# Optimization experiments

Measured on AMD Instinct MI355X. Metric: run time of the kernel, lower is better.

The kernel has to match this reference:

```python
import jax, jax.numpy as jnp
import numpy as np

NUM_HEADS = 16

def setup_inputs() -> dict:
    key = jax.random.key(0)
    ks = jax.random.split(key, 5)
    B, N, C = 2, 2048, 1024
    x = jax.random.normal(ks[0], (B, N, C), dtype=jnp.float32)
    s_in = 1.0 / np.sqrt(C)
    Wq = jax.random.normal(ks[1], (C, 2 * C), dtype=jnp.float32) * s_in
    Wk = jax.random.normal(ks[2], (C, 2 * C), dtype=jnp.float32) * s_in
    Wv = jax.random.normal(ks[3], (C, 2 * C), dtype=jnp.float32) * s_in
    Wo = jax.random.normal(ks[4], (2 * C, C), dtype=jnp.float32) * (1.0 / np.sqrt(2 * C))
    return {"x": x, "Wq": Wq, "Wk": Wk, "Wv": Wv, "Wo": Wo}

def reference(x, Wq, Wk, Wv, Wo):
    B, N, C = x.shape
    H = NUM_HEADS
    hd = C // H  # head_dim
    def proj(W):
        # [B,N,2C] -> [B,H,N,2*hd]
        return (x @ W).reshape(B, N, H, 2 * hd).transpose(0, 2, 1, 3)
    q = proj(Wq)
    k = proj(Wk)
    v = proj(Wv)
    q_r, q_i = q[..., :hd], q[..., hd:]
    k_r, k_i = k[..., :hd], k[..., hd:]
    v_r, v_i = v[..., :hd], v[..., hd:]
    # complex inner product real part: Re(Q K^H) = q_r.k_r + q_i.k_i
    scores = (jnp.einsum('bhnd,bhmd->bhnm', q_r, k_r)
              + jnp.einsum('bhnd,bhmd->bhnm', q_i, k_i)) / jnp.sqrt(jnp.float32(hd))
    causal = jnp.tril(jnp.ones((N, N), dtype=bool))  # [N,N]
    scores = jnp.where(causal[None, None], scores, -jnp.inf)
    probs = jax.nn.softmax(scores, axis=-1)  # dropout off (eval mode)
    out_r = jnp.einsum('bhnm,bhmd->bhnd', probs, v_r)
    out_i = jnp.einsum('bhnm,bhmd->bhnd', probs, v_i)
    out = jnp.concatenate([out_r, out_i], axis=-1)  # [B,H,N,2*hd]
    out = out.transpose(0, 2, 1, 3).reshape(B, N, 2 * C)
    return out @ Wo  # [B,N,C]
```

## Files before the change

### kernel.cpp

```cpp
#include <hip/hip_runtime.h>
#include <hip/hip_bf16.h>
#include <stdint.h>
#include <cmath>

using bf16 = __hip_bfloat16;
typedef __attribute__((ext_vector_type(8))) short bf16x8;
typedef __attribute__((ext_vector_type(4))) short bf16x4;
typedef __attribute__((ext_vector_type(4))) float f32x4;

#define MFMA16(a, b, c) __builtin_amdgcn_mfma_f32_16x16x32_bf16(a, b, c, 0, 0, 0)

#if defined(__has_builtin)
#if __has_builtin(__builtin_amdgcn_mfma_f32_16x16x16bf16_1k)
#define HAVE_MFMA_K16 1
#endif
#if __has_builtin(__builtin_amdgcn_exp2f)
#define EXP2F __builtin_amdgcn_exp2f
#endif
#endif
#ifndef HAVE_MFMA_K16
#define HAVE_MFMA_K16 0
#endif
#ifndef EXP2F
#define EXP2F exp2f
#endif

#define NEG_BIG (-1e30f)
#define K2SCALE 0.18033688011112042f

__device__ __forceinline__ short f2bf(float v) {
  return __builtin_bit_cast(short, __float2bfloat16(v));
}

__device__ __forceinline__ f32x4 pv_mfma(bf16x4 va, bf16x4 pb, f32x4 c) {
#if HAVE_MFMA_K16
  return __builtin_amdgcn_mfma_f32_16x16x16bf16_1k(va, pb, c, 0, 0, 0);
#else
  const bf16x8 a = {va[0], va[1], va[2], va[3], 0, 0, 0, 0};
  const bf16x8 b = {pb[0], pb[1], pb[2], pb[3], 0, 0, 0, 0};
  return MFMA16(a, b, c);
#endif
}

__device__ __forceinline__ void async_ld16(const bf16* g, bf16* l) {
  __builtin_amdgcn_global_load_lds(
      (const __attribute__((address_space(1))) unsigned int*)g,
      (__attribute__((address_space(3))) unsigned int*)l, 16, 0, 0);
}

template <typename T> __device__ __forceinline__ T cvt_out(float v);
template <> __device__ __forceinline__ float cvt_out<float>(float v) { return v; }
template <> __device__ __forceinline__ bf16 cvt_out<bf16>(float v) { return __float2bfloat16(v); }

__global__ void prep(const float* __restrict__ x,
                     const float* __restrict__ Wq, const float* __restrict__ Wk,
                     const float* __restrict__ Wv, const float* __restrict__ Wo,
                     bf16* __restrict__ xb, bf16* __restrict__ tq,
                     bf16* __restrict__ tk, bf16* __restrict__ tv,
                     bf16* __restrict__ to_) {
  __shared__ bf16 tile[32][33];
  const int bid = blockIdx.x;
  if (bid < 8192) {
    const int z = bid >> 11, tt = bid & 2047;
    const float* in = z == 0 ? Wq : z == 1 ? Wk : z == 2 ? Wv : Wo;
    bf16* out = z == 0 ? tq : z == 1 ? tk : z == 2 ? tv : to_;
    int R, Cc, c0, r0;
    if (z < 3) { R = 1024; Cc = 2048; c0 = (tt & 63) * 32; r0 = (tt >> 6) * 32; }
    else       { R = 2048; Cc = 1024; c0 = (tt & 31) * 32; r0 = (tt >> 5) * 32; }
    const int xx = threadIdx.x & 31;
    const int y = threadIdx.x >> 5;
#pragma unroll
    for (int yy = y; yy < 32; yy += 8)
      tile[yy][xx] = __float2bfloat16(in[(size_t)(r0 + yy) * Cc + c0 + xx]);
    __syncthreads();
#pragma unroll
    for (int yy = y; yy < 32; yy += 8)
      out[(size_t)(c0 + yy) * R + r0 + xx] = tile[xx][yy];
  } else {
    const int i = (bid - 8192) * 256 + threadIdx.x;
    const float4 v = ((const float4*)x)[i];
    bf16 o[4] = {__float2bfloat16(v.x), __float2bfloat16(v.y),
                 __float2bfloat16(v.z), __float2bfloat16(v.w)};
    *(uint64_t*)&xb[i * 4] = *(const uint64_t*)o;
  }
}

__global__ __launch_bounds__(256)
void gemm_qkv(const bf16* __restrict__ xb, const bf16* __restrict__ wq,
              const bf16* __restrict__ wk, const bf16* __restrict__ wv,
              bf16* __restrict__ qo, bf16* __restrict__ ko, bf16* __restrict__ vo) {
  __shared__ __align__(16) bf16 As[128 * 32];
  __shared__ __align__(16) bf16 Bs[128 * 32];
  const int op = blockIdx.y;
  const int bid = blockIdx.x;
  const bf16 *A, *B;
  int m0, n0;
  if (op < 2) { A = xb; B = op ? wk : wq; m0 = (bid >> 4) * 128; n0 = (bid & 15) * 128; }
  else        { A = wv; B = xb;           m0 = (bid & 15) * 128; n0 = (bid >> 4) * 128; }
  const int K = 1024;

  const int t = threadIdx.x;
  const int l = t & 63, w = t >> 6;
  const int q4 = l >> 4, li = l & 15;
  const int wr = (w >> 1) * 64, wc = (w & 1) * 64;

  f32x4 acc[4][4] = {};
  const int colst = (t & 3) * 8;
  const bf16* gA = A + (size_t)m0 * K;
  const bf16* gB = B + (size_t)n0 * K;

  for (int k0 = 0; k0 < K; k0 += 32) {
#pragma unroll
    for (int p = 0; p < 2; ++p) {
      const int row = p * 64 + (t >> 2);
      const int lbase = p * 2048 + (t & ~63) * 8;
      async_ld16(gA + (size_t)row * K + k0 + colst, &As[lbase]);
      async_ld16(gB + (size_t)row * K + k0 + colst, &Bs[lbase]);
    }
    __syncthreads();
    bf16x8 af[4], bfr[4];
#pragma unroll
    for (int i = 0; i < 4; ++i)
      af[i] = *(const bf16x8*)&As[(wr + i * 16 + li) * 32 + q4 * 8];
#pragma unroll
    for (int j = 0; j < 4; ++j)
      bfr[j] = *(const bf16x8*)&Bs[(wc + j * 16 + li) * 32 + q4 * 8];
#pragma unroll
    for (int i = 0; i < 4; ++i)
#pragma unroll
      for (int j = 0; j < 4; ++j)
        acc[i][j] = MFMA16(af[i], bfr[j], acc[i][j]);
    __syncthreads();
  }

#pragma unroll
  for (int i = 0; i < 4; ++i)
#pragma unroll
    for (int j = 0; j < 4; ++j)
#pragma unroll
      for (int r = 0; r < 4; ++r) {
        const int gm = m0 + wr + i * 16 + q4 * 4 + r;
        const int gn = n0 + wc + j * 16 + li;
        const bf16 v = __float2bfloat16(acc[i][j][r]);
        if (op < 2) {
          const int b = gm >> 11, nn = gm & 2047;
          const int h = gn >> 7, d = gn & 127;
          (op ? ko : qo)[((size_t)(b * 16 + h) * 2048 + nn) * 128 + d] = v;
        } else {
          const int h = gm >> 7, d = gm & 127;
          const int b = gn >> 11, nn = gn & 2047;
          vo[((size_t)(b * 16 + h) * 128 + d) * 2048 + nn] = v;
        }
      }
}

template <int NT, typename OT>
__global__ __launch_bounds__(256)
void gemm_bt(const bf16* __restrict__ A, const bf16* __restrict__ B,
             OT* __restrict__ C, int M, int N, int K) {
  __shared__ __align__(16) bf16 As[128 * 32];
  __shared__ __align__(16) bf16 Bs[NT * 32];
  constexpr int JN = NT / 32;
  const int t = threadIdx.x;
  const int l = t & 63, w = t >> 6;
  const int q4 = l >> 4, li = l & 15;
  const int m0 = blockIdx.y * 128;
  const int n0 = blockIdx.x * NT;
  const int wr = (w >> 1) * 64, wc = (w & 1) * (NT / 2);

  f32x4 acc[4][JN] = {};
  const int colst = (t & 3) * 8;
  const bf16* gA = A + (size_t)m0 * K;
  const bf16* gB = B + (size_t)n0 * K;

  for (int k0 = 0; k0 < K; k0 += 32) {
#pragma unroll
    for (int p = 0; p < 2; ++p) {
      const int row = p * 64 + (t >> 2);
      const int lbase = p * 2048 + (t & ~63) * 8;
      async_ld16(gA + (size_t)row * K + k0 + colst, &As[lbase]);
    }
#pragma unroll
    for (int p = 0; p < NT / 64; ++p) {
      const int row = p * 64 + (t >> 2);
      const int lbase = p * 2048 + (t & ~63) * 8;
      async_ld16(gB + (size_t)row * K + k0 + colst, &Bs[lbase]);
    }
    __syncthreads();
    bf16x8 af[4], bfr[JN];
#pragma unroll
    for (int i = 0; i < 4; ++i)
      af[i] = *(const bf16x8*)&As[(wr + i * 16 + li) * 32 + q4 * 8];
#pragma unroll
    for (int j = 0; j < JN; ++j)
      bfr[j] = *(const bf16x8*)&Bs[(wc + j * 16 + li) * 32 + q4 * 8];
#pragma unroll
    for (int i = 0; i < 4; ++i)
#pragma unroll
      for (int j = 0; j < JN; ++j)
        acc[i][j] = MFMA16(af[i], bfr[j], acc[i][j]);
    __syncthreads();
  }

#pragma unroll
  for (int i = 0; i < 4; ++i)
#pragma unroll
    for (int j = 0; j < JN; ++j)
#pragma unroll
      for (int r = 0; r < 4; ++r) {
        const int gm = m0 + wr + i * 16 + q4 * 4 + r;
        const int gn = n0 + wc + j * 16 + li;
        C[(size_t)gm * N + gn] = cvt_out<OT>(acc[i][j][r]);
      }
}

__global__ __launch_bounds__(256, 2)
void flash_attn(const bf16* __restrict__ qm, const bf16* __restrict__ km,
                const bf16* __restrict__ vtm, bf16* __restrict__ om) {
  __shared__ __align__(16) bf16 Ks[128 * 128];
  __shared__ __align__(16) bf16 Vts[128 * 128];

  const int t = threadIdx.x;
  const int l = t & 63, w = t >> 6;
  const int q4 = l >> 4, li = l & 15;
  const int bh = blockIdx.x;
  const int y = blockIdx.y;
  const int qt = (y < 8) ? 15 - y : y - 8;
  const int qs = qt * 128;
  const size_t qkbase = (size_t)bh * 2048 * 128;
  const size_t vbase = (size_t)bh * 128 * 2048;
  const int b = bh >> 4, h = bh & 15;

  bf16x8 qf[2][4];
#pragma unroll
  for (int g = 0; g < 2; ++g) {
    const bf16* Qb = qm + qkbase + (size_t)(qs + w * 32 + g * 16 + li) * 128;
#pragma unroll
    for (int f = 0; f < 4; ++f)
      qf[g][f] = *(const bf16x8*)(Qb + f * 32 + q4 * 8);
  }

  f32x4 O[2][8] = {};
  float mrun[2] = {NEG_BIG, NEG_BIG}, lrun[2] = {0.f, 0.f};
  const int gmq[2] = {qs + w * 32 + li, qs + w * 32 + 16 + li};

  const int srow = t >> 4;
  const int wavebase = (t & ~63) * 8;

  for (int kt = 0; kt <= qt; ++kt) {
    const int kn = kt * 128;
#pragma unroll
    for (int p = 0; p < 8; ++p) {
      const int row = p * 16 + srow;
      const int cs = (t & 15) ^ (row & 7);
      const int ldsoff = p * 2048 + wavebase;
      async_ld16(km + qkbase + (size_t)(kn + row) * 128 + cs * 8, &Ks[ldsoff]);
      async_ld16(vtm + vbase + (size_t)row * 2048 + kn + cs * 8, &Vts[ldsoff]);
    }
    __syncthreads();

    const bool diag = (kt == qt);
#pragma unroll
    for (int half = 0; half < 2; ++half) {
      const int kb = kn + half * 64;
      if (diag && (qs + w * 32 + 31) < kb) continue;

      f32x4 S[2][4];
#pragma unroll
      for (int jk = 0; jk < 4; ++jk) {
        const int krow = half * 64 + jk * 16 + li;
        bf16x8 kf[4];
#pragma unroll
        for (int f = 0; f < 4; ++f)
          kf[f] = *(const bf16x8*)&Ks[krow * 128 + (((f * 4 + q4) ^ (li & 7)) * 8)];
#pragma unroll
        for (int g = 0; g < 2; ++g) {
          f32x4 s = {0.f, 0.f, 0.f, 0.f};
#pragma unroll
          for (int f = 0; f < 4; ++f) s = MFMA16(kf[f], qf[g][f], s);
          S[g][jk] = s;
        }
      }

      bf16x4 pb[2][4];
      float mold[2], nmv[2], rsv[2];
      bool nomove = true;
#pragma unroll
      for (int g = 0; g < 2; ++g) {
        if (diag) {
#pragma unroll
          for (int jk = 0; jk < 4; ++jk)
#pragma unroll
            for (int r = 0; r < 4; ++r)
              if ((kb + jk * 16 + q4 * 4 + r) > gmq[g]) S[g][jk][r] = NEG_BIG;
        }
        float mx = NEG_BIG;
#pragma unroll
        for (int jk = 0; jk < 4; ++jk)
          mx = fmaxf(mx, fmaxf(fmaxf(S[g][jk][0], S[g][jk][1]),
                               fmaxf(S[g][jk][2], S[g][jk][3])));
        mx = fmaxf(mx, __shfl_xor(mx, 16));
        mx = fmaxf(mx, __shfl_xor(mx, 32));
        mold[g] = mrun[g];
        const float nm = fmaxf(mrun[g], mx);
        nomove = nomove && (mx <= mold[g]);
        mrun[g] = nm;
        nmv[g] = nm;
        const float nmk = nm * K2SCALE;
        float rs = 0.f;
#pragma unroll
        for (int jk = 0; jk < 4; ++jk)
#pragma unroll
          for (int r = 0; r < 4; ++r) {
            const float e = EXP2F(__builtin_fmaf(S[g][jk][r], K2SCALE, -nmk));
            rs += e;
            pb[g][jk][r] = f2bf(e);
          }
        rs += __shfl_xor(rs, 16);
        rs += __shfl_xor(rs, 32);
        rsv[g] = rs;
      }

      if (__all(nomove)) {
        lrun[0] += rsv[0];
        lrun[1] += rsv[1];
      } else {
#pragma unroll
        for (int g = 0; g < 2; ++g) {
          const float alpha = EXP2F((mold[g] - nmv[g]) * K2SCALE);
          lrun[g] = lrun[g] * alpha + rsv[g];
#pragma unroll
          for (int dt = 0; dt < 8; ++dt) O[g][dt] *= alpha;
        }
      }

#pragma unroll
      for (int dt = 0; dt < 8; ++dt)
#pragma unroll
        for (int kc = 0; kc < 4; ++kc) {
          const int gchunk = half * 8 + kc * 2 + (q4 >> 1);
          const bf16x4 va = *(const bf16x4*)&Vts[(dt * 16 + li) * 128 +
                                                 ((gchunk ^ (li & 7)) * 8) +
                                                 (q4 & 1) * 4];
          O[0][dt] = pv_mfma(va, pb[0][kc], O[0][dt]);
          O[1][dt] = pv_mfma(va, pb[1][kc], O[1][dt]);
        }
    }
    __syncthreads();
  }

#pragma unroll
  for (int g = 0; g < 2; ++g) {
    const float inv = 1.0f / lrun[g];
    const size_t orow = (size_t)(b * 2048 + qs + w * 32 + g * 16 + li) * 2048 + h * 128;
#pragma unroll
    for (int dt = 0; dt < 8; ++dt) {
      bf16x4 o4;
#pragma unroll
      for (int r = 0; r < 4; ++r) o4[r] = f2bf(O[g][dt][r] * inv);
      *(bf16x4*)&om[orow + dt * 16 + q4 * 4] = o4;
    }
  }
}

extern "C" void kernel_launch(void* const* d_in, const int* in_sizes, int n_in,
                              void* d_out, int out_size, void* d_ws, size_t ws_size,
                              hipStream_t stream) {
  const float* x = (const float*)d_in[0];
  const float* Wq = (const float*)d_in[1];
  const float* Wk = (const float*)d_in[2];
  const float* Wv = (const float*)d_in[3];
  const float* Wo = (const float*)d_in[4];
  float* out = (float*)d_out;

  bf16* ws = (bf16*)d_ws;
  const size_t MEG = 1u << 20;
  bf16* xb = ws;
  bf16* wTq = ws + 4 * MEG;
  bf16* wTk = ws + 6 * MEG;
  bf16* wTv = ws + 8 * MEG;
  bf16* woT = ws + 10 * MEG;
  bf16* at_ws = ws + 2 * MEG;
  bf16* q_ws = ws + 12 * MEG;
  bf16* k_ws = ws + 20 * MEG;
  bf16* vt_ws = ws + 28 * MEG;

  const dim3 blk(256);

  prep<<<dim3(12288), blk, 0, stream>>>(x, Wq, Wk, Wv, Wo, xb, wTq, wTk, wTv, woT);
  gemm_qkv<<<dim3(512, 3), blk, 0, stream>>>(xb, wTq, wTk, wTv, q_ws, k_ws, vt_ws);
  flash_attn<<<dim3(32, 16), blk, 0, stream>>>(q_ws, k_ws, vt_ws, at_ws);
  gemm_bt<64, float><<<dim3(16, 32), blk, 0, stream>>>(at_ws, woT, out, 4096, 1024, 2048);
}
```

Measured before the change: 273.9 us.

## Double-buffer 64-key K/V tiles to overlap global loads with attention compute

Splits each 128-key KV tile into 64-key tiles held in two LDS buffers, so the async loads for the next tile are issued while the current tile is being computed. The old code issued all loads and then waited at a barrier, leaving compute idle. LDS footprint stays the same, but there are twice as many barriers, and the V tile indexing and swizzle now use a 64-column layout.

Result: slower. 280.7 us (+2.5%).

```diff
diff --git a/kernel.cpp b/kernel.cpp
--- a/kernel.cpp
+++ b/kernel.cpp
@@ -217,8 +217,8 @@
 __global__ __launch_bounds__(256, 2)
 void flash_attn(const bf16* __restrict__ qm, const bf16* __restrict__ km,
                 const bf16* __restrict__ vtm, bf16* __restrict__ om) {
-  __shared__ __align__(16) bf16 Ks[128 * 128];
-  __shared__ __align__(16) bf16 Vts[128 * 128];
+  __shared__ __align__(16) bf16 Ks[2][64 * 128];
+  __shared__ __align__(16) bf16 Vts[2][128 * 64];
 
   const int t = threadIdx.x;
   const int l = t & 63, w = t >> 6;
@@ -244,35 +244,60 @@
   float mrun[2] = {NEG_BIG, NEG_BIG}, lrun[2] = {0.f, 0.f};
   const int gmq[2] = {qs + w * 32 + li, qs + w * 32 + 16 + li};
 
-  const int srow = t >> 4;
+  const int ksrow = t >> 4;
+  const int kchu = t & 15;
+  const int vsrow = t >> 3;
+  const int vchu = t & 7;
   const int wavebase = (t & ~63) * 8;
 
-  for (int kt = 0; kt <= qt; ++kt) {
-    const int kn = kt * 128;
-#pragma unroll
-    for (int p = 0; p < 8; ++p) {
-      const int row = p * 16 + srow;
-      const int cs = (t & 15) ^ (row & 7);
-      const int ldsoff = p * 2048 + wavebase;
-      async_ld16(km + qkbase + (size_t)(kn + row) * 128 + cs * 8, &Ks[ldsoff]);
-      async_ld16(vtm + vbase + (size_t)row * 2048 + kn + cs * 8, &Vts[ldsoff]);
-    }
-    __syncthreads();
-
-    const bool diag = (kt == qt);
-#pragma unroll
-    for (int half = 0; half < 2; ++half) {
-      const int kb = kn + half * 64;
-      if (diag && (qs + w * 32 + 31) < kb) continue;
+  const int nt = 2 * qt + 2;
+
+  {
+#pragma unroll
+    for (int p = 0; p < 4; ++p) {
+      const int kr = p * 16 + ksrow;
+      async_ld16(km + qkbase + (size_t)kr * 128 + (size_t)((kchu ^ (kr & 7)) * 8),
+                 &Ks[0][p * 2048 + wavebase]);
+      const int vr = p * 32 + vsrow;
+      async_ld16(vtm + vbase + (size_t)vr * 2048 + (size_t)((vchu ^ (vr & 7)) * 8),
+                 &Vts[0][p * 2048 + wavebase]);
+    }
+  }
+  asm volatile("s_waitcnt vmcnt(0)" ::: "memory");
+  __builtin_amdgcn_s_barrier();
+  asm volatile("" ::: "memory");
+
+  int cur = 0;
+  for (int j = 0; j < nt; ++j, cur ^= 1) {
+    if (j + 1 < nt) {
+      const int kn = (j + 1) * 64;
+      bf16* kd = &Ks[cur ^ 1][0];
+      bf16* vd = &Vts[cur ^ 1][0];
+#pragma unroll
+      for (int p = 0; p < 4; ++p) {
+        const int kr = p * 16 + ksrow;
+        async_ld16(km + qkbase + (size_t)(kn + kr) * 128 + (size_t)((kchu ^ (kr & 7)) * 8),
+                   kd + p * 2048 + wavebase);
+        const int vr = p * 32 + vsrow;
+        async_ld16(vtm + vbase + (size_t)vr * 2048 + kn + (size_t)((vchu ^ (vr & 7)) * 8),
+                   vd + p * 2048 + wavebase);
+      }
+    }
+
+    const int kb = j * 64;
+    if (!((qs + w * 32 + 31) < kb)) {
+      const bool msk = (j >= 2 * qt);
+      const bf16* Kc = &Ks[cur][0];
+      const bf16* Vc = &Vts[cur][0];
 
       f32x4 S[2][4];
 #pragma unroll
       for (int jk = 0; jk < 4; ++jk) {
-        const int krow = half * 64 + jk * 16 + li;
+        const int krow = jk * 16 + li;
         bf16x8 kf[4];
 #pragma unroll
         for (int f = 0; f < 4; ++f)
-          kf[f] = *(const bf16x8*)&Ks[krow * 128 + (((f * 4 + q4) ^ (li & 7)) * 8)];
+          kf[f] = *(const bf16x8*)&Kc[krow * 128 + (((f * 4 + q4) ^ (li & 7)) * 8)];
 #pragma unroll
         for (int g = 0; g < 2; ++g) {
           f32x4 s = {0.f, 0.f, 0.f, 0.f};
@@ -287,7 +312,7 @@
       bool nomove = true;
 #pragma unroll
       for (int g = 0; g < 2; ++g) {
-        if (diag) {
+        if (msk) {
 #pragma unroll
           for (int jk = 0; jk < 4; ++jk)
 #pragma unroll
@@ -338,15 +363,18 @@
       for (int dt = 0; dt < 8; ++dt)
 #pragma unroll
         for (int kc = 0; kc < 4; ++kc) {
-          const int gchunk = half * 8 + kc * 2 + (q4 >> 1);
-          const bf16x4 va = *(const bf16x4*)&Vts[(dt * 16 + li) * 128 +
-                                                 ((gchunk ^ (li & 7)) * 8) +
-                                                 (q4 & 1) * 4];
+          const int gc = kc * 2 + (q4 >> 1);
+          const bf16x4 va = *(const bf16x4*)&Vc[(dt * 16 + li) * 64 +
+                                                ((gc ^ (li & 7)) * 8) +
+                                                (q4 & 1) * 4];
           O[0][dt] = pv_mfma(va, pb[0][kc], O[0][dt]);
           O[1][dt] = pv_mfma(va, pb[1][kc], O[1][dt]);
         }
     }
-    __syncthreads();
+
+    asm volatile("s_waitcnt vmcnt(0) lgkmcnt(0)" ::: "memory");
+    __builtin_amdgcn_s_barrier();
+    asm volatile("" ::: "memory");
   }
 
 #pragma unroll
```

## Halve flash-attention KV tile to 64 keys and raise occupancy hint to 4

Applied to the files above, without the earlier changes.

Changes the flash-attention loop to stage 64-key K and V^T tiles in shared memory instead of 128, cutting LDS use per block in half, and raises the launch-bounds minimum blocks per CU from 2 to 4. The aim is more resident blocks to hide global-load latency. The cost is twice as many loop iterations and barriers per query tile, and the tighter register budget may cause spills given the large O accumulator.

Result: slower. 363.6 us (+32.7%).

```diff
diff --git a/kernel.cpp b/kernel.cpp
--- a/kernel.cpp
+++ b/kernel.cpp
@@ -214,11 +214,11 @@
       }
 }
 
-__global__ __launch_bounds__(256, 2)
+__global__ __launch_bounds__(256, 4)
 void flash_attn(const bf16* __restrict__ qm, const bf16* __restrict__ km,
                 const bf16* __restrict__ vtm, bf16* __restrict__ om) {
-  __shared__ __align__(16) bf16 Ks[128 * 128];
-  __shared__ __align__(16) bf16 Vts[128 * 128];
+  __shared__ __align__(16) bf16 Ks[64 * 128];
+  __shared__ __align__(16) bf16 Vts[128 * 64];
 
   const int t = threadIdx.x;
   const int l = t & 63, w = t >> 6;
@@ -244,31 +244,34 @@
   float mrun[2] = {NEG_BIG, NEG_BIG}, lrun[2] = {0.f, 0.f};
   const int gmq[2] = {qs + w * 32 + li, qs + w * 32 + 16 + li};
 
-  const int srow = t >> 4;
+  const int ksrow = t >> 4;
+  const int kchu = t & 15;
+  const int vsrow = t >> 3;
+  const int vchu = t & 7;
   const int wavebase = (t & ~63) * 8;
 
-  for (int kt = 0; kt <= qt; ++kt) {
-    const int kn = kt * 128;
-#pragma unroll
-    for (int p = 0; p < 8; ++p) {
-      const int row = p * 16 + srow;
-      const int cs = (t & 15) ^ (row & 7);
-      const int ldsoff = p * 2048 + wavebase;
-      async_ld16(km + qkbase + (size_t)(kn + row) * 128 + cs * 8, &Ks[ldsoff]);
-      async_ld16(vtm + vbase + (size_t)row * 2048 + kn + cs * 8, &Vts[ldsoff]);
-    }
-    __syncthreads();
-
-    const bool diag = (kt == qt);
-#pragma unroll
-    for (int half = 0; half < 2; ++half) {
-      const int kb = kn + half * 64;
-      if (diag && (qs + w * 32 + 31) < kb) continue;
+  const int nt = 2 * qt + 2;
+
+  for (int j = 0; j < nt; ++j) {
+    const int kb = j * 64;
+#pragma unroll
+    for (int p = 0; p < 4; ++p) {
+      const int kr = p * 16 + ksrow;
+      async_ld16(km + qkbase + (size_t)(kb + kr) * 128 + (size_t)((kchu ^ (kr & 7)) * 8),
+                 &Ks[p * 2048 + wavebase]);
+      const int vr = p * 32 + vsrow;
+      async_ld16(vtm + vbase + (size_t)vr * 2048 + kb + (size_t)((vchu ^ (vr & 7)) * 8),
+                 &Vts[p * 2048 + wavebase]);
+    }
+    __syncthreads();
+
+    if (!((qs + w * 32 + 31) < kb)) {
+      const bool msk = (j >= 2 * qt);
 
       f32x4 S[2][4];
 #pragma unroll
       for (int jk = 0; jk < 4; ++jk) {
-        const int krow = half * 64 + jk * 16 + li;
+        const int krow = jk * 16 + li;
         bf16x8 kf[4];
 #pragma unroll
         for (int f = 0; f < 4; ++f)
@@ -287,7 +290,7 @@
       bool nomove = true;
 #pragma unroll
       for (int g = 0; g < 2; ++g) {
-        if (diag) {
+        if (msk) {
 #pragma unroll
           for (int jk = 0; jk < 4; ++jk)
 #pragma unroll
@@ -338,9 +341,9 @@
       for (int dt = 0; dt < 8; ++dt)
 #pragma unroll
         for (int kc = 0; kc < 4; ++kc) {
-          const int gchunk = half * 8 + kc * 2 + (q4 >> 1);
-          const bf16x4 va = *(const bf16x4*)&Vts[(dt * 16 + li) * 128 +
-                                                 ((gchunk ^ (li & 7)) * 8) +
+          const int gc = kc * 2 + (q4 >> 1);
+          const bf16x4 va = *(const bf16x4*)&Vts[(dt * 16 + li) * 64 +
+                                                 ((gc ^ (li & 7)) * 8) +
                                                  (q4 & 1) * 4];
           O[0][dt] = pv_mfma(va, pb[0][kc], O[0][dt]);
           O[1][dt] = pv_mfma(va, pb[1][kc], O[1][dt]);
```
